# Kernel tuning notes

Measured on AMD Instinct MI355X. Metric: run time of the kernel, lower is better.

The kernel has to match this reference:

```python
import jax, jax.numpy as jnp
import numpy as np

N_NODES = 100000
N_EDGES = 1600000
IN_CH = 128
HID = 128
OUT_CH = 10


def setup_inputs() -> dict:
    key = jax.random.key(0)
    ks = jax.random.split(key, 14)
    s_in = 1.0 / np.sqrt(IN_CH)
    s_h = 1.0 / np.sqrt(HID)
    return {
        "x0": jax.random.normal(ks[0], (N_NODES, IN_CH), jnp.float32),
        "edge_index": jax.random.randint(ks[1], (2, N_EDGES), 0, N_NODES, jnp.int32),
        "edge_weight": jax.random.uniform(ks[2], (N_EDGES,), jnp.float32),
        # GraphConv layer 1 (in -> hid): lin_rel (weight+bias) applied to aggregated msgs, lin_root (no bias)
        "W1_rel": jax.random.uniform(ks[3], (IN_CH, HID), jnp.float32, -s_in, s_in),
        "b1": jax.random.uniform(ks[4], (HID,), jnp.float32, -s_in, s_in),
        "W1_root": jax.random.uniform(ks[5], (IN_CH, HID), jnp.float32, -s_in, s_in),
        # GraphConv layer 2 (hid -> hid)
        "W2_rel": jax.random.uniform(ks[6], (HID, HID), jnp.float32, -s_h, s_h),
        "b2": jax.random.uniform(ks[7], (HID,), jnp.float32, -s_h, s_h),
        "W2_root": jax.random.uniform(ks[8], (HID, HID), jnp.float32, -s_h, s_h),
        # GraphConv layer 3 (hid -> hid)
        "W3_rel": jax.random.uniform(ks[9], (HID, HID), jnp.float32, -s_h, s_h),
        "b3": jax.random.uniform(ks[10], (HID,), jnp.float32, -s_h, s_h),
        "W3_root": jax.random.uniform(ks[11], (HID, HID), jnp.float32, -s_h, s_h),
        # classification head
        "W_lin": jax.random.uniform(ks[12], (HID, OUT_CH), jnp.float32, -s_h, s_h),
        "b_lin": jax.random.uniform(ks[13], (OUT_CH,), jnp.float32, -s_h, s_h),
    }


def _graph_conv(x, src, dst, ew, W_rel, b_rel, W_root):
    # message: x_j * w_e ; aggregate: scatter-add onto dst ; update: lin_rel(agg) + lin_root(x)
    msg = x[src] * ew[:, None]                                   # [E, C]
    agg = jax.ops.segment_sum(msg, dst, num_segments=x.shape[0])  # [N, C]
    return agg @ W_rel + b_rel + x @ W_root                      # [N, C']


def reference(x0, edge_index, edge_weight,
              W1_rel, b1, W1_root,
              W2_rel, b2, W2_root,
              W3_rel, b3, W3_root,
              W_lin, b_lin):
    src, dst = edge_index[0], edge_index[1]
    # dropout p=0.2 is identity in eval mode
    x1 = jax.nn.relu(_graph_conv(x0, src, dst, edge_weight, W1_rel, b1, W1_root))
    x2 = jax.nn.relu(_graph_conv(x1, src, dst, edge_weight, W2_rel, b2, W2_root))
    x3 = jax.nn.relu(_graph_conv(x2, src, dst, edge_weight, W3_rel, b3, W3_root))
    logits = x3 @ W_lin + b_lin
    return jax.nn.log_softmax(logits, axis=-1)
```

## Files before the change

kernel.cpp:

```cpp
#include <hip/hip_runtime.h>
#include <hip/hip_bf16.h>
#include <math.h>

#define C128 128
#define OUT_CH 10

typedef __attribute__((ext_vector_type(8))) short short8;
typedef __attribute__((ext_vector_type(4))) float f32x4;
typedef __attribute__((ext_vector_type(2))) float f32x2;
typedef __attribute__((ext_vector_type(4))) int i32x4;

__device__ __forceinline__ unsigned short f2bf(float f) {
    unsigned b = __float_as_uint(f);
    unsigned r = (b + 0x7FFF + ((b >> 16) & 1)) >> 16;
    return (unsigned short)r;
}
__device__ __forceinline__ float bf2f(unsigned short u) {
    return __uint_as_float(((unsigned)u) << 16);
}


#define NBMAX 400
#define BCAP  4608
#define P1K   4096


__global__ __launch_bounds__(512) void prep_kernel(
    const int* __restrict__ ei, const float* __restrict__ ew,
    int* __restrict__ gcur, unsigned* __restrict__ bins_rec,
    unsigned char* __restrict__ bins_dst, int E, int nb, int binBlocks,
    const float4* __restrict__ x, ushort4* __restrict__ xb,
    unsigned* __restrict__ xf8, int n4, int cvtBlocks,
    const float* __restrict__ W1r, const float* __restrict__ W1t,
    const float* __restrict__ W2r, const float* __restrict__ W2t,
    const float* __restrict__ W3r, const float* __restrict__ W3t,
    const float* __restrict__ Wl,
    unsigned short* __restrict__ Wp1, unsigned short* __restrict__ Wp2,
    unsigned short* __restrict__ Wp3, unsigned short* __restrict__ WlP)
{
    __shared__ int cnt[NBMAX];
    __shared__ int pos[NBMAX];
    __shared__ int gbase[NBMAX];
    __shared__ int s[512];
    __shared__ int totalSh;
    __shared__ uint2 buf[P1K];

    const int blk = blockIdx.x;
    const int t = threadIdx.x;

    if (blk >= binBlocks) {
        int b2 = blk - binBlocks;
        if (b2 < cvtBlocks) {
            int i = b2 * 512 + t;
            if (i < n4) {
                float4 v = x[i];
                ushort4 o;
                o.x = f2bf(v.x); o.y = f2bf(v.y); o.z = f2bf(v.z); o.w = f2bf(v.w);
                xb[i] = o;
                unsigned p = __builtin_amdgcn_cvt_pk_fp8_f32(v.x, v.y, 0, false);
                p = __builtin_amdgcn_cvt_pk_fp8_f32(v.z, v.w, p, true);
                xf8[i] = p;
            }
        } else {
            int idx = (b2 - cvtBlocks) * 512 + t;
            if (idx < 3 * 32768) {
                int which = idx >> 15;
                int lx = idx & 32767;
                const float* Wr = (which == 0) ? W1r : (which == 1) ? W2r : W3r;
                const float* Wt = (which == 0) ? W1t : (which == 1) ? W2t : W3t;
                unsigned short* Wp = (which == 0) ? Wp1 : (which == 1) ? Wp2 : Wp3;
                int j    = lx & 7;
                int n    = (lx >> 3) & 127;
                int quad = (lx >> 10) & 3;
                int ks   = lx >> 12;
                const float* W = (ks < 4) ? Wr : Wt;
                int k = (ks & 3) * 32 + quad * 8 + j;
                Wp[lx] = f2bf(W[(size_t)k * C128 + n]);
            } else if (idx < 3 * 32768 + 4096) {
                int lx = idx - 3 * 32768;
                int j    = lx & 7;
                int col  = (lx >> 3) & 15;
                int quad = (lx >> 7) & 3;
                int ks   = (lx >> 9) & 3;
                int half = lx >> 11;
                int k = ks * 32 + quad * 8 + j;
                float v = (col < OUT_CH) ? Wl[(size_t)k * OUT_CH + col] : 0.f;
                unsigned short hi = f2bf(v);
                unsigned short outv = hi;
                if (half) outv = f2bf(v - bf2f(hi));
                WlP[lx] = outv;
            }
        }
        return;
    }

    const int e0 = blk * P1K;

    for (int b = t; b < nb; b += 512) { cnt[b] = 0; pos[b] = 0; }
    __syncthreads();

    unsigned rec[8];
    int dstv[8];
    const int e = e0 + t * 8;
    if (e + 8 <= E) {
        i32x4 d0 = __builtin_nontemporal_load((const i32x4*)(ei + E + e));
        i32x4 d1 = __builtin_nontemporal_load((const i32x4*)(ei + E + e + 4));
        i32x4 s0 = __builtin_nontemporal_load((const i32x4*)(ei + e));
        i32x4 s1 = __builtin_nontemporal_load((const i32x4*)(ei + e + 4));
        f32x4 w0 = __builtin_nontemporal_load((const f32x4*)(ew + e));
        f32x4 w1 = __builtin_nontemporal_load((const f32x4*)(ew + e + 4));
        int dd[8] = {d0.x, d0.y, d0.z, d0.w, d1.x, d1.y, d1.z, d1.w};
        int ss[8] = {s0.x, s0.y, s0.z, s0.w, s1.x, s1.y, s1.z, s1.w};
        float ww[8] = {w0.x, w0.y, w0.z, w0.w, w1.x, w1.y, w1.z, w1.w};
#pragma unroll
        for (int j = 0; j < 8; ++j) {
            unsigned wb = __float_as_uint(ww[j]);
            unsigned r  = ((wb + 0x7FFF + ((wb >> 16) & 1)) >> 16) & 0x7FFFu;
            rec[j]  = (unsigned)ss[j] | (r << 17);
            dstv[j] = dd[j];
            atomicAdd(&cnt[dd[j] >> 8], 1);
        }
    } else {
#pragma unroll
        for (int j = 0; j < 8; ++j) {
            int ee = e + j;
            if (ee < E) {
                int dst = ei[E + ee];
                unsigned wb = __float_as_uint(ew[ee]);
                unsigned r  = ((wb + 0x7FFF + ((wb >> 16) & 1)) >> 16) & 0x7FFFu;
                rec[j]  = (unsigned)ei[ee] | (r << 17);
                dstv[j] = dst;
                atomicAdd(&cnt[dst >> 8], 1);
            } else {
                dstv[j] = -1;
            }
        }
    }
    __syncthreads();

    int c = (t < nb) ? cnt[t] : 0;
    s[t] = c;
    __syncthreads();
    for (int o = 1; o < 512; o <<= 1) {
        int u = (t >= o) ? s[t - o] : 0;
        __syncthreads();
        s[t] += u;
        __syncthreads();
    }
    if (t == nb - 1) totalSh = s[t];
    __syncthreads();

#pragma unroll
    for (int j = 0; j < 8; ++j) {
        if (dstv[j] >= 0) {
            int b = dstv[j] >> 8;
            int r = atomicAdd(&pos[b], 1);
            buf[s[b] - cnt[b] + r] = make_uint2(rec[j], (unsigned)dstv[j]);
        }
    }
    __syncthreads();

    if (t < nb) {
        int b = t + (int)((blk * 131u) % (unsigned)nb);
        if (b >= nb) b -= nb;
        int cb = cnt[b];
        if (cb > 0) gbase[b] = atomicAdd(&gcur[b], cb);
    }
    __syncthreads();

    const int total = totalSh;
    for (int i = t; i < total; i += 512) {
        uint2 v = buf[i];
        int b = (int)(v.y >> 8);
        int dest = gbase[b] + (i - (s[b] - cnt[b]));
        if (dest < BCAP) {
            bins_rec[(size_t)b * BCAP + dest] = v.x;
            bins_dst[(size_t)b * BCAP + dest] = (unsigned char)(v.y & 255u);
        }
    }
}


__global__ __launch_bounds__(256) void build_kernel(
    const unsigned* __restrict__ bins_rec, const unsigned char* __restrict__ bins_dst,
    const int* __restrict__ gcur, int* __restrict__ row_ptr,
    unsigned* __restrict__ csr, int N, int nb)
{
    __shared__ int rowCnt[256];
    __shared__ int rowOff[256];
    __shared__ int sc[256];
    __shared__ unsigned out[BCAP];
    __shared__ int baseSh;

    const int b = blockIdx.x, t = threadIdx.x;

    int a0 = (2 * t < nb) ? gcur[2 * t] : 0;
    int a1 = (2 * t + 1 < nb) ? gcur[2 * t + 1] : 0;
    sc[t] = a0 + a1;
    __syncthreads();
    for (int o = 1; o < 256; o <<= 1) {
        int u = (t >= o) ? sc[t - o] : 0;
        __syncthreads();
        sc[t] += u;
        __syncthreads();
    }
    if (t == (b >> 1)) {
        int excl = sc[t] - (a0 + a1);
        baseSh = excl + ((b & 1) ? a0 : 0);
    }
    __syncthreads();
    const int base = baseSh;

    int cnt = gcur[b];
    if (cnt > BCAP) cnt = BCAP;
    const unsigned* mbr = bins_rec + (size_t)b * BCAP;
    const unsigned char* mbd = bins_dst + (size_t)b * BCAP;

    rowCnt[t] = 0;
    __syncthreads();
    for (int i = t; i < cnt; i += 256) atomicAdd(&rowCnt[(int)mbd[i]], 1);
    __syncthreads();

    int v = rowCnt[t];
    sc[t] = v;
    __syncthreads();
    for (int o = 1; o < 256; o <<= 1) {
        int u = (t >= o) ? sc[t - o] : 0;
        __syncthreads();
        sc[t] += u;
        __syncthreads();
    }
    rowOff[t] = sc[t] - v;
    int idx = b * 256 + t;
    if (idx <= N) row_ptr[idx] = base + sc[t] - v;
    rowCnt[t] = 0;
    __syncthreads();

    for (int i = t; i < cnt; i += 256) {
        int d = (int)mbd[i];
        int k = atomicAdd(&rowCnt[d], 1);
        out[rowOff[d] + k] = mbr[i];
    }
    __syncthreads();

    for (int i = t; i < cnt; i += 256) csr[base + i] = out[i];
}


#define AGS 136

#define GATHER_BODY(rec_, rem_, acc2_)                                          \
    for (int c = 0; c < (rem_); c += 16) {                                      \
        int i0e = c + g, i1e = c + 4 + g, i2e = c + 8 + g, i3e = c + 12 + g;    \
        int s0 = __shfl((rec_), i0e & 63, 64);                                  \
        int s1 = __shfl((rec_), i1e & 63, 64);                                  \
        int s2 = __shfl((rec_), i2e & 63, 64);                                  \
        int s3 = __shfl((rec_), i3e & 63, 64);                                  \
        float w0 = (i0e < (rem_)) ? __uint_as_float(((unsigned)s0 >> 17) << 16) : 0.f; \
        float w1 = (i1e < (rem_)) ? __uint_as_float(((unsigned)s1 >> 17) << 16) : 0.f; \
        float w2 = (i2e < (rem_)) ? __uint_as_float(((unsigned)s2 >> 17) << 16) : 0.f; \
        float w3 = (i3e < (rem_)) ? __uint_as_float(((unsigned)s3 >> 17) << 16) : 0.f; \
        uint2 q0 = *(const uint2*)&xf8[(unsigned)(s0 & 0x1FFFF) * 32u + l16 * 2]; \
        uint2 q1 = *(const uint2*)&xf8[(unsigned)(s1 & 0x1FFFF) * 32u + l16 * 2]; \
        uint2 q2 = *(const uint2*)&xf8[(unsigned)(s2 & 0x1FFFF) * 32u + l16 * 2]; \
        uint2 q3 = *(const uint2*)&xf8[(unsigned)(s3 & 0x1FFFF) * 32u + l16 * 2]; \
        { f32x2 w2v = {w0, w0};                                                 \
          (acc2_)[0] += __builtin_amdgcn_cvt_pk_f32_fp8(q0.x, false) * w2v;     \
          (acc2_)[1] += __builtin_amdgcn_cvt_pk_f32_fp8(q0.x, true)  * w2v;     \
          (acc2_)[2] += __builtin_amdgcn_cvt_pk_f32_fp8(q0.y, false) * w2v;     \
          (acc2_)[3] += __builtin_amdgcn_cvt_pk_f32_fp8(q0.y, true)  * w2v; }   \
        { f32x2 w2v = {w1, w1};                                                 \
          (acc2_)[0] += __builtin_amdgcn_cvt_pk_f32_fp8(q1.x, false) * w2v;     \
          (acc2_)[1] += __builtin_amdgcn_cvt_pk_f32_fp8(q1.x, true)  * w2v;     \
          (acc2_)[2] += __builtin_amdgcn_cvt_pk_f32_fp8(q1.y, false) * w2v;     \
          (acc2_)[3] += __builtin_amdgcn_cvt_pk_f32_fp8(q1.y, true)  * w2v; }   \
        { f32x2 w2v = {w2, w2};                                                 \
          (acc2_)[0] += __builtin_amdgcn_cvt_pk_f32_fp8(q2.x, false) * w2v;     \
          (acc2_)[1] += __builtin_amdgcn_cvt_pk_f32_fp8(q2.x, true)  * w2v;     \
          (acc2_)[2] += __builtin_amdgcn_cvt_pk_f32_fp8(q2.y, false) * w2v;     \
          (acc2_)[3] += __builtin_amdgcn_cvt_pk_f32_fp8(q2.y, true)  * w2v; }   \
        { f32x2 w2v = {w3, w3};                                                 \
          (acc2_)[0] += __builtin_amdgcn_cvt_pk_f32_fp8(q3.x, false) * w2v;     \
          (acc2_)[1] += __builtin_amdgcn_cvt_pk_f32_fp8(q3.x, true)  * w2v;     \
          (acc2_)[2] += __builtin_amdgcn_cvt_pk_f32_fp8(q3.y, false) * w2v;     \
          (acc2_)[3] += __builtin_amdgcn_cvt_pk_f32_fp8(q3.y, true)  * w2v; }   \
    }

#define GATHER_PHASE                                                            \
    if (w < 4) {                                                                \
        int rrow = tile0 + w * 4 + g;                                           \
        int srow = (rrow < N) ? rrow : 0;                                       \
        uint4 v = *(const uint4*)&xb[(size_t)srow * C128 + l16 * 8];            \
        *(uint4*)&XR[(w * 4 + g) * AGS + l16 * 8] = v;                          \
    }                                                                           \
    int pi0[2], pdeg[2], prec[2];                                               \
    _Pragma("unroll")                                                           \
    for (int i = 0; i < 2; ++i) {                                               \
        int node = tile0 + w * 2 + i;                                           \
        int a = 0, d = 0;                                                       \
        if (node < N) { a = row_ptr[node]; d = row_ptr[node + 1] - a; }         \
        pi0[i] = a; pdeg[i] = d;                                                \
    }                                                                           \
    _Pragma("unroll")                                                           \
    for (int i = 0; i < 2; ++i) {                                               \
        prec[i] = 0;                                                            \
        if (lane < pdeg[i])                                                     \
            prec[i] = (int)__builtin_nontemporal_load(&csr[pi0[i] + lane]);     \
    }                                                                           \
    _Pragma("unroll")                                                           \
    for (int i = 0; i < 2; ++i) {                                               \
        int deg = pdeg[i];                                                      \
        f32x2 acc2[4];                                                          \
        acc2[0] = acc2[1] = acc2[2] = acc2[3] = (f32x2){0.f, 0.f};              \
        int rem0 = (deg < 64) ? deg : 64;                                       \
        GATHER_BODY(prec[i], rem0, acc2)                                        \
        for (int base = 64; base < deg; base += 64) {                           \
            int rem = deg - base; if (rem > 64) rem = 64;                       \
            int rec = 0;                                                        \
            if (base + lane < deg)                                              \
                rec = (int)__builtin_nontemporal_load(&csr[pi0[i] + base + lane]); \
            GATHER_BODY(rec, rem, acc2)                                         \
        }                                                                       \
        _Pragma("unroll")                                                       \
        for (int j = 0; j < 4; ++j) {                                           \
            acc2[j].x += __shfl_xor(acc2[j].x, 16, 64);                         \
            acc2[j].y += __shfl_xor(acc2[j].y, 16, 64);                         \
            acc2[j].x += __shfl_xor(acc2[j].x, 32, 64);                         \
            acc2[j].y += __shfl_xor(acc2[j].y, 32, 64);                         \
        }                                                                       \
        if (g == 0) {                                                           \
            uint4 o;                                                            \
            o.x = (unsigned)f2bf(acc2[0].x) | ((unsigned)f2bf(acc2[0].y) << 16); \
            o.y = (unsigned)f2bf(acc2[1].x) | ((unsigned)f2bf(acc2[1].y) << 16); \
            o.z = (unsigned)f2bf(acc2[2].x) | ((unsigned)f2bf(acc2[2].y) << 16); \
            o.w = (unsigned)f2bf(acc2[3].x) | ((unsigned)f2bf(acc2[3].y) << 16); \
            *(uint4*)&AG[(w * 2 + i) * AGS + l16 * 8] = o;                      \
        }                                                                       \
    }

__global__ __launch_bounds__(512) void fused_layer(
    const unsigned* __restrict__ xf8,
    const int* __restrict__ row_ptr,
    const unsigned* __restrict__ csr,
    const unsigned short* __restrict__ xb,
    const unsigned short* __restrict__ Wp,
    const float* __restrict__ bias,
    unsigned short* __restrict__ outb, unsigned char* __restrict__ outf8, int N)
{
    __shared__ unsigned short AG[16 * AGS];
    __shared__ unsigned short XR[16 * AGS];

    const int t = threadIdx.x;
    const int w    = t >> 6;
    const int lane = t & 63;
    const int l16  = lane & 15;
    const int g    = lane >> 4;
    const int tile0 = blockIdx.x * 16;

    GATHER_PHASE
    __syncthreads();

    const int l15 = l16, quad = g;
    const int nt = w;
    float bv = bias[nt * 16 + l15];
    f32x4 acc = (f32x4){0.f, 0.f, 0.f, 0.f};

#pragma unroll
    for (int ks = 0; ks < 8; ++ks) {
        short8 a;
        if (ks < 4) a = *(const short8*)&AG[l15 * AGS + ks * 32 + quad * 8];
        else        a = *(const short8*)&XR[l15 * AGS + (ks - 4) * 32 + quad * 8];
        short8 b = *(const short8*)&Wp[(((ks * 4 + quad) * 128) + nt * 16 + l15) * 8];
        acc = __builtin_amdgcn_mfma_f32_16x16x32_bf16(a, b, acc, 0, 0, 0);
    }

#pragma unroll
    for (int r = 0; r < 4; ++r) {
        int row = tile0 + quad * 4 + r;
        if (row < N) {
            float v = fmaxf(acc[r] + bv, 0.f);
            outb[(size_t)row * C128 + nt * 16 + l15] = f2bf(v);
            unsigned p8 = __builtin_amdgcn_cvt_pk_fp8_f32(v, 0.f, 0, false);
            outf8[(size_t)row * C128 + nt * 16 + l15] = (unsigned char)(p8 & 0xff);
        }
    }
}

__global__ __launch_bounds__(512) void fused_layer_head(
    const unsigned* __restrict__ xf8,
    const int* __restrict__ row_ptr,
    const unsigned* __restrict__ csr,
    const unsigned short* __restrict__ xb,
    const unsigned short* __restrict__ Wp,
    const float* __restrict__ bias,
    const unsigned short* __restrict__ WlP, const float* __restrict__ bl,
    float* __restrict__ out, int N)
{
    __shared__ unsigned short AG[16 * AGS];
    __shared__ unsigned short XR[16 * AGS];

    const int t = threadIdx.x;
    const int w    = t >> 6;
    const int lane = t & 63;
    const int l16  = lane & 15;
    const int g    = lane >> 4;
    const int tile0 = blockIdx.x * 16;

    GATHER_PHASE
    __syncthreads();

    const int l15 = l16, quad = g;
    const int nt = w;
    float bv = bias[nt * 16 + l15];
    f32x4 acc = (f32x4){0.f, 0.f, 0.f, 0.f};

#pragma unroll
    for (int ks = 0; ks < 8; ++ks) {
        short8 a;
        if (ks < 4) a = *(const short8*)&AG[l15 * AGS + ks * 32 + quad * 8];
        else        a = *(const short8*)&XR[l15 * AGS + (ks - 4) * 32 + quad * 8];
        short8 b = *(const short8*)&Wp[(((ks * 4 + quad) * 128) + nt * 16 + l15) * 8];
        acc = __builtin_amdgcn_mfma_f32_16x16x32_bf16(a, b, acc, 0, 0, 0);
    }

    __syncthreads();
#pragma unroll
    for (int r = 0; r < 4; ++r) {
        int lrow = quad * 4 + r;
        float v = fmaxf(acc[r] + bv, 0.f);
        AG[lrow * AGS + nt * 16 + l15] = f2bf(v);
    }
    __syncthreads();

    if (w == 0) {
        f32x4 hacc = (f32x4){0.f, 0.f, 0.f, 0.f};
#pragma unroll
        for (int ks = 0; ks < 4; ++ks) {
            short8 a2  = *(const short8*)&AG[l15 * AGS + ks * 32 + quad * 8];
            short8 bh  = *(const short8*)&WlP[(((ks * 4 + quad) * 16) + l15) * 8];
            short8 bl2 = *(const short8*)&WlP[2048 + (((ks * 4 + quad) * 16) + l15) * 8];
            hacc = __builtin_amdgcn_mfma_f32_16x16x32_bf16(a2, bh, hacc, 0, 0, 0);
            hacc = __builtin_amdgcn_mfma_f32_16x16x32_bf16(a2, bl2, hacc, 0, 0, 0);
        }
        float blv = (l15 < OUT_CH) ? bl[l15] : 0.f;
#pragma unroll
        for (int r = 0; r < 4; ++r) {
            int row = tile0 + quad * 4 + r;
            float lg = (l15 < OUT_CH) ? (hacc[r] + blv) : -1e30f;
            float m = lg;
            m = fmaxf(m, __shfl_xor(m, 1, 64));
            m = fmaxf(m, __shfl_xor(m, 2, 64));
            m = fmaxf(m, __shfl_xor(m, 4, 64));
            m = fmaxf(m, __shfl_xor(m, 8, 64));
            float s = __expf(lg - m);
            s += __shfl_xor(s, 1, 64);
            s += __shfl_xor(s, 2, 64);
            s += __shfl_xor(s, 4, 64);
            s += __shfl_xor(s, 8, 64);
            float lse = m + __logf(s);
            if (l15 < OUT_CH && row < N)
                out[(size_t)row * OUT_CH + l15] = lg - lse;
        }
    }
}


extern "C" void kernel_launch(void* const* d_in, const int* in_sizes, int n_in,
                              void* d_out, int out_size, void* d_ws, size_t ws_size,
                              hipStream_t stream) {
    const float* x0   = (const float*)d_in[0];
    const int*   ei   = (const int*)  d_in[1];
    const float* ew   = (const float*)d_in[2];
    const float* W1r  = (const float*)d_in[3];
    const float* b1   = (const float*)d_in[4];
    const float* W1t  = (const float*)d_in[5];
    const float* W2r  = (const float*)d_in[6];
    const float* b2   = (const float*)d_in[7];
    const float* W2t  = (const float*)d_in[8];
    const float* W3r  = (const float*)d_in[9];
    const float* b3   = (const float*)d_in[10];
    const float* W3t  = (const float*)d_in[11];
    const float* Wlin = (const float*)d_in[12];
    const float* blin = (const float*)d_in[13];

    const int N = in_sizes[0] / C128;
    const int E = in_sizes[1] / 2;
    const int nb = (N + 255) >> 8;
    const int n4 = N * C128 / 4;

    char* ws = (char*)d_ws;
    size_t off = 0;
    auto alloc = [&](size_t bytes) {
        void* p = ws + off;
        off = (off + bytes + 255) & ~(size_t)255;
        return p;
    };
    size_t bb = (size_t)N * C128 * sizeof(unsigned short);
    size_t fb = (size_t)N * C128;
    unsigned short* xb0  = (unsigned short*)alloc(bb);
    unsigned short* xb1  = (unsigned short*)alloc(bb);
    unsigned char*  xf8a = (unsigned char*)alloc(fb);
    unsigned char*  xf8b = (unsigned char*)alloc(fb);
    unsigned short* Wp1  = (unsigned short*)alloc(32768 * 2);
    unsigned short* Wp2  = (unsigned short*)alloc(32768 * 2);
    unsigned short* Wp3  = (unsigned short*)alloc(32768 * 2);
    unsigned short* WlP  = (unsigned short*)alloc(4096 * 2);
    unsigned* csr  = (unsigned*)alloc((size_t)E * 4);
    int* row_ptr   = (int*)alloc((size_t)(N + 2) * 4);
    unsigned* bins_rec  = (unsigned*)alloc((size_t)nb * BCAP * 4);
    unsigned char* bins_dst = (unsigned char*)alloc((size_t)nb * BCAP);
    int* gcur      = (int*)alloc((size_t)nb * 4);

    const int binBlocks = (E + P1K - 1) / P1K;
    const int cvtBlocks = (n4 + 511) / 512;
    const int packBlocks = (3 * 32768 + 4096 + 511) / 512;
    const int prepGrid = binBlocks + cvtBlocks + packBlocks;

    hipMemsetAsync(gcur, 0, (size_t)nb * sizeof(int), stream);
    prep_kernel<<<prepGrid, 512, 0, stream>>>(
        ei, ew, gcur, bins_rec, bins_dst, E, nb, binBlocks,
        (const float4*)x0, (ushort4*)xb0, (unsigned*)xf8a, n4, cvtBlocks,
        W1r, W1t, W2r, W2t, W3r, W3t, Wlin, Wp1, Wp2, Wp3, WlP);

    build_kernel<<<nb, 256, 0, stream>>>(bins_rec, bins_dst, gcur, row_ptr, csr, N, nb);

    const int fusedGrid = (N + 15) / 16;

    fused_layer<<<fusedGrid, 512, 0, stream>>>(
        (const unsigned*)xf8a, row_ptr, csr, xb0, Wp1, b1, xb1, xf8b, N);
    fused_layer<<<fusedGrid, 512, 0, stream>>>(
        (const unsigned*)xf8b, row_ptr, csr, xb1, Wp2, b2, xb0, xf8a, N);
    fused_layer_head<<<fusedGrid, 512, 0, stream>>>(
        (const unsigned*)xf8a, row_ptr, csr, xb0, Wp3, b3, WlP, blin,
        (float*)d_out, N);
}
```

Before: 353.9 us.

## Widen CSR build blocks to 512 threads and split fused layers into two launches

The CSR build kernel now runs 512 threads per block, with only the first 256 doing the scans and the full 512 striding over edges for counting and scattering. Each fused GraphConv layer is split into two half-grid launches with a tile offset on the same stream. The launch split looks like a probe of launch granularity or cache locality rather than a real overlap, since launches on one stream still serialize. It adds launch overhead and a drain gap between halves.

Result: no change. 360.1 us (+1.7%).

```diff
diff --git a/kernel.cpp b/kernel.cpp
--- a/kernel.cpp
+++ b/kernel.cpp
@@ -181,7 +181,7 @@
 }
 
 
-__global__ __launch_bounds__(256) void build_kernel(
+__global__ __launch_bounds__(512) void build_kernel(
     const unsigned* __restrict__ bins_rec, const unsigned char* __restrict__ bins_dst,
     const int* __restrict__ gcur, int* __restrict__ row_ptr,
     unsigned* __restrict__ csr, int N, int nb)
@@ -194,14 +194,17 @@
 
     const int b = blockIdx.x, t = threadIdx.x;
 
-    int a0 = (2 * t < nb) ? gcur[2 * t] : 0;
-    int a1 = (2 * t + 1 < nb) ? gcur[2 * t + 1] : 0;
-    sc[t] = a0 + a1;
+    int a0 = 0, a1 = 0;
+    if (t < 256) {
+        a0 = (2 * t < nb) ? gcur[2 * t] : 0;
+        a1 = (2 * t + 1 < nb) ? gcur[2 * t + 1] : 0;
+        sc[t] = a0 + a1;
+    }
     __syncthreads();
     for (int o = 1; o < 256; o <<= 1) {
-        int u = (t >= o) ? sc[t - o] : 0;
+        int u = (t < 256 && t >= o) ? sc[t - o] : 0;
         __syncthreads();
-        sc[t] += u;
+        if (t < 256) sc[t] += u;
         __syncthreads();
     }
     if (t == (b >> 1)) {
@@ -216,34 +219,36 @@
     const unsigned* mbr = bins_rec + (size_t)b * BCAP;
     const unsigned char* mbd = bins_dst + (size_t)b * BCAP;
 
-    rowCnt[t] = 0;
-    __syncthreads();
-    for (int i = t; i < cnt; i += 256) atomicAdd(&rowCnt[(int)mbd[i]], 1);
-    __syncthreads();
-
-    int v = rowCnt[t];
-    sc[t] = v;
+    if (t < 256) rowCnt[t] = 0;
+    __syncthreads();
+    for (int i = t; i < cnt; i += 512) atomicAdd(&rowCnt[(int)mbd[i]], 1);
+    __syncthreads();
+
+    int v = 0;
+    if (t < 256) { v = rowCnt[t]; sc[t] = v; }
     __syncthreads();
     for (int o = 1; o < 256; o <<= 1) {
-        int u = (t >= o) ? sc[t - o] : 0;
+        int u = (t < 256 && t >= o) ? sc[t - o] : 0;
         __syncthreads();
-        sc[t] += u;
+        if (t < 256) sc[t] += u;
         __syncthreads();
     }
-    rowOff[t] = sc[t] - v;
-    int idx = b * 256 + t;
-    if (idx <= N) row_ptr[idx] = base + sc[t] - v;
-    rowCnt[t] = 0;
-    __syncthreads();
-
-    for (int i = t; i < cnt; i += 256) {
+    if (t < 256) {
+        rowOff[t] = sc[t] - v;
+        int idx = b * 256 + t;
+        if (idx <= N) row_ptr[idx] = base + sc[t] - v;
+        rowCnt[t] = 0;
+    }
+    __syncthreads();
+
+    for (int i = t; i < cnt; i += 512) {
         int d = (int)mbd[i];
         int k = atomicAdd(&rowCnt[d], 1);
         out[rowOff[d] + k] = mbr[i];
     }
     __syncthreads();
 
-    for (int i = t; i < cnt; i += 256) csr[base + i] = out[i];
+    for (int i = t; i < cnt; i += 512) csr[base + i] = out[i];
 }
 
 
@@ -345,7 +350,8 @@
     const unsigned short* __restrict__ xb,
     const unsigned short* __restrict__ Wp,
     const float* __restrict__ bias,
-    unsigned short* __restrict__ outb, unsigned char* __restrict__ outf8, int N)
+    unsigned short* __restrict__ outb, unsigned char* __restrict__ outf8,
+    int N, int tileOff)
 {
     __shared__ unsigned short AG[16 * AGS];
     __shared__ unsigned short XR[16 * AGS];
@@ -355,7 +361,7 @@
     const int lane = t & 63;
     const int l16  = lane & 15;
     const int g    = lane >> 4;
-    const int tile0 = blockIdx.x * 16;
+    const int tile0 = (blockIdx.x + tileOff) * 16;
 
     GATHER_PHASE
     __syncthreads();
@@ -394,7 +400,7 @@
     const unsigned short* __restrict__ Wp,
     const float* __restrict__ bias,
     const unsigned short* __restrict__ WlP, const float* __restrict__ bl,
-    float* __restrict__ out, int N)
+    float* __restrict__ out, int N, int tileOff)
 {
     __shared__ unsigned short AG[16 * AGS];
     __shared__ unsigned short XR[16 * AGS];
@@ -404,7 +410,7 @@
     const int lane = t & 63;
     const int l16  = lane & 15;
     const int g    = lane >> 4;
-    const int tile0 = blockIdx.x * 16;
+    const int tile0 = (blockIdx.x + tileOff) * 16;
 
     GATHER_PHASE
     __syncthreads();
@@ -522,15 +528,24 @@
         (const float4*)x0, (ushort4*)xb0, (unsigned*)xf8a, n4, cvtBlocks,
         W1r, W1t, W2r, W2t, W3r, W3t, Wlin, Wp1, Wp2, Wp3, WlP);
 
-    build_kernel<<<nb, 256, 0, stream>>>(bins_rec, bins_dst, gcur, row_ptr, csr, N, nb);
+    build_kernel<<<nb, 512, 0, stream>>>(bins_rec, bins_dst, gcur, row_ptr, csr, N, nb);
 
     const int fusedGrid = (N + 15) / 16;
-
-    fused_layer<<<fusedGrid, 512, 0, stream>>>(
-        (const unsigned*)xf8a, row_ptr, csr, xb0, Wp1, b1, xb1, xf8b, N);
-    fused_layer<<<fusedGrid, 512, 0, stream>>>(
-        (const unsigned*)xf8b, row_ptr, csr, xb1, Wp2, b2, xb0, xf8a, N);
-    fused_layer_head<<<fusedGrid, 512, 0, stream>>>(
+    const int hA = (fusedGrid + 1) / 2;
+    const int hB = fusedGrid - hA;
+
+    fused_layer<<<hA, 512, 0, stream>>>(
+        (const unsigned*)xf8a, row_ptr, csr, xb0, Wp1, b1, xb1, xf8b, N, 0);
+    fused_layer<<<hB, 512, 0, stream>>>(
+        (const unsigned*)xf8a, row_ptr, csr, xb0, Wp1, b1, xb1, xf8b, N, hA);
+    fused_layer<<<hA, 512, 0, stream>>>(
+        (const unsigned*)xf8b, row_ptr, csr, xb1, Wp2, b2, xb0, xf8a, N, 0);
+    fused_layer<<<hB, 512, 0, stream>>>(
+        (const unsigned*)xf8b, row_ptr, csr, xb1, Wp2, b2, xb0, xf8a, N, hA);
+    fused_layer_head<<<hA, 512, 0, stream>>>(
         (const unsigned*)xf8a, row_ptr, csr, xb0, Wp3, b3, WlP, blin,
-        (float*)d_out, N);
-}
+        (float*)d_out, N, 0);
+    fused_layer_head<<<hB, 512, 0, stream>>>(
+        (const unsigned*)xf8a, row_ptr, csr, xb0, Wp3, b3, WlP, blin,
+        (float*)d_out, N, hA);
+}
```
